# Kernel tuning notes

Measured on AMD Instinct MI355X. Metric: run time of the kernel, lower is better.

## Reference

```python
import jax, jax.numpy as jnp
import numpy as np


def _gla_forward(hidden_state, Wq, bq, Wk, bk, Wv, bv, Wg, bg, Wo, bo):
    # hidden_state: (B, T, H)
    q = hidden_state @ Wq + bq                       # (B, T, K)
    k = jax.nn.sigmoid(hidden_state @ Wk + bk)       # (B, T, K)
    g = jax.nn.sigmoid(hidden_state @ Wg + bg)       # (B, T, K)
    v = hidden_state @ Wv + bv                       # (B, T, V)

    B = hidden_state.shape[0]
    K = Wq.shape[1]
    V = Wv.shape[1]
    state0 = jnp.zeros((B, K, V), dtype=hidden_state.dtype)

    def step(state, inp):
        q_t, k_t, g_t, v_t = inp                     # (B,K),(B,K),(B,K),(B,V)
        # state = state * gate[..., None] + k outer v
        state = state * g_t[:, :, None] + k_t[:, :, None] * v_t[:, None, :]
        out_t = jnp.einsum('bkv,bk->bv', state, q_t)  # (B, V)
        return state, out_t

    # scan over time: move T to leading axis
    xs = (jnp.swapaxes(q, 0, 1), jnp.swapaxes(k, 0, 1),
          jnp.swapaxes(g, 0, 1), jnp.swapaxes(v, 0, 1))
    final_state, outs = jax.lax.scan(step, state0, xs)  # outs: (T, B, V)
    out = jnp.swapaxes(outs, 0, 1)                      # (B, T, V)
    out = out @ Wo + bo                                 # (B, T, O)
    return out, final_state


def setup_inputs() -> dict:
    key = jax.random.key(0)
    ks = jax.random.split(key, 12)
    B, T, H, K, V, O = 8, 2048, 1024, 256, 256, 1024
    s = 0.02
    return {
        'hidden_state': jax.random.normal(ks[0], (B, T, H), dtype=jnp.float32),
        'Wq': jax.random.normal(ks[1], (H, K), dtype=jnp.float32) * s,
        'bq': jax.random.normal(ks[2], (K,), dtype=jnp.float32) * s,
        'Wk': jax.random.normal(ks[3], (H, K), dtype=jnp.float32) * s,
        'bk': jax.random.normal(ks[4], (K,), dtype=jnp.float32) * s,
        'Wv': jax.random.normal(ks[5], (H, V), dtype=jnp.float32) * s,
        'bv': jax.random.normal(ks[6], (V,), dtype=jnp.float32) * s,
        'Wg': jax.random.normal(ks[7], (H, K), dtype=jnp.float32) * s,
        'bg': jax.random.normal(ks[8], (K,), dtype=jnp.float32) * s,
        'Wo': jax.random.normal(ks[9], (V, O), dtype=jnp.float32) * s,
        'bo': jax.random.normal(ks[10], (O,), dtype=jnp.float32) * s,
    }


def reference(hidden_state, Wq, bq, Wk, bk, Wv, bv, Wg, bg, Wo, bo):
    return _gla_forward(hidden_state, Wq, bq, Wk, bk, Wv, bv, Wg, bg, Wo, bo)
```

## Files before the change

kernel.cpp:

```cpp
#include <hip/hip_runtime.h>

#define Bb 8
#define Tt 2048
#define Hh 1024
#define Kk 256
#define Vv 256
#define Oo 1024
#define CC 64
#define NC 32

typedef __attribute__((ext_vector_type(8))) __bf16 bf16x8;
typedef __attribute__((ext_vector_type(4))) float f32x4;

__device__ __forceinline__ unsigned short f2b(float f) {
  unsigned u = __float_as_uint(f);
  u = (u + 0x7FFFu + ((u >> 16) & 1u)) >> 16;
  return (unsigned short)u;
}
__device__ __forceinline__ float b2f(unsigned short u) {
  return __uint_as_float(((unsigned)u) << 16);
}
__device__ __forceinline__ void gload_lds16(const unsigned short* g, unsigned short* l) {
  __builtin_amdgcn_global_load_lds(
      (const __attribute__((address_space(1))) void*)g,
      (__attribute__((address_space(3))) void*)l, 16, 0, 0);
}

__global__ __launch_bounds__(256) void cast_bf16_kernel(const float* __restrict__ in,
                                                        unsigned short* __restrict__ out,
                                                        int n4) {
  int i = blockIdx.x * 256 + threadIdx.x;
  if (i >= n4) return;
  float4 v = ((const float4*)in)[i];
  ushort4 o;
  o.x = f2b(v.x); o.y = f2b(v.y); o.z = f2b(v.z); o.w = f2b(v.w);
  ((ushort4*)out)[i] = o;
}

__global__ __launch_bounds__(256) void transpose_cast_kernel(const float* __restrict__ W,
                                                             unsigned short* __restrict__ WT,
                                                             int H, int N) {
  __shared__ float tile[32][33];
  int h0 = blockIdx.x * 32, n0 = blockIdx.y * 32;
  int tx = threadIdx.x & 31, ty = threadIdx.x >> 5;
  for (int r = ty; r < 32; r += 8)
    tile[r][tx] = W[(size_t)(h0 + r) * N + n0 + tx];
  __syncthreads();
  for (int r = ty; r < 32; r += 8)
    WT[(size_t)(n0 + r) * H + h0 + tx] = f2b(tile[tx][r]);
}

__global__ __launch_bounds__(256) void transpose_b16_kernel(
    const unsigned short* __restrict__ in, unsigned short* __restrict__ out,
    int R, int C) {
  __shared__ unsigned short tile[32][33];
  const int r0 = blockIdx.x * 32, c0 = blockIdx.y * 32;
  const size_t base = (size_t)blockIdx.z * R * C;
  const int tx = threadIdx.x & 31, ty = threadIdx.x >> 5;
  for (int rr = ty; rr < 32; rr += 8)
    tile[rr][tx] = in[base + (size_t)(r0 + rr) * C + c0 + tx];
  __syncthreads();
  for (int rr = ty; rr < 32; rr += 8)
    out[base + (size_t)(c0 + rr) * R + r0 + tx] = tile[tx][rr];
}

#define BM 128
#define BN 128
#define BK 64

template <int MODE>
__global__ __launch_bounds__(256, 4) void gemm_mf_kernel(
    const unsigned short* __restrict__ A, const unsigned short* __restrict__ Bt,
    const float* __restrict__ b0p, const float* __restrict__ b1p,
    const float* __restrict__ b2p, const float* __restrict__ b3p,
    float* __restrict__ Cf,
    unsigned short* __restrict__ O0, unsigned short* __restrict__ O1,
    unsigned short* __restrict__ O2, unsigned short* __restrict__ O3,
    int M, int N, int K) {
  __shared__ __align__(16) unsigned short As[BM * BK];
  __shared__ __align__(16) unsigned short Bs[BN * BK];
  const int tid = threadIdx.x;
  const int lane = tid & 63, wid = tid >> 6;
  const int wm = wid >> 1, wn = wid & 1;
  const int lin = blockIdx.x + blockIdx.y * gridDim.x;
  const int cpx = (gridDim.x * gridDim.y) >> 3;
  const int swz = (lin & 7) * cpx + (lin >> 3);
  const int m0 = (swz / gridDim.x) * BM, n0 = (swz % gridDim.x) * BN;
  const int fr = lane & 15, fq = lane >> 4;
  const int srl = lane >> 3;
  const int scs = ((lane & 7) ^ srl) * 8;
  const unsigned short* gaBase = A + (size_t)(m0 + srl) * K + scs;
  const unsigned short* gbBase = Bt + (size_t)(n0 + srl) * K + scs;

  f32x4 acc[4][4] = {};
  const int nt = K / BK;
  for (int t = 0; t < nt; ++t) {
    const int k0 = t * BK;
    __syncthreads();
#pragma unroll
    for (int inst = 0; inst < 4; ++inst) {
      const int rb = wid * 32 + inst * 8;
      gload_lds16(gaBase + (size_t)rb * K + k0, &As[rb * BK]);
      gload_lds16(gbBase + (size_t)rb * K + k0, &Bs[rb * BK]);
    }
    __syncthreads();
#pragma unroll
    for (int ks = 0; ks < 2; ++ks) {
      bf16x8 af[4], bfv[4];
#pragma unroll
      for (int j = 0; j < 4; ++j) {
        const int R = wn * 64 + j * 16 + fr;
        const int ch = ((ks << 2) | fq) ^ (fr & 7);
        bfv[j] = *(const bf16x8*)&Bs[R * BK + ch * 8];
      }
#pragma unroll
      for (int i = 0; i < 4; ++i) {
        const int R = wm * 64 + i * 16 + fr;
        const int ch = ((ks << 2) | fq) ^ (fr & 7);
        af[i] = *(const bf16x8*)&As[R * BK + ch * 8];
      }
#pragma unroll
      for (int i = 0; i < 4; ++i)
#pragma unroll
        for (int j = 0; j < 4; ++j)
          acc[i][j] = __builtin_amdgcn_mfma_f32_16x16x32_bf16(af[i], bfv[j], acc[i][j], 0, 0, 0);
    }
  }
  if (MODE == 1) {
#pragma unroll
    for (int j = 0; j < 4; ++j) {
      const int n = n0 + wn * 64 + j * 16 + fr;
      const float bv = b0p[n];
#pragma unroll
      for (int i = 0; i < 4; ++i) {
        const int mb = m0 + wm * 64 + i * 16 + fq * 4;
#pragma unroll
        for (int r = 0; r < 4; ++r)
          Cf[(size_t)(mb + r) * N + n] = acc[i][j][r] + bv;
      }
    }
  } else {
    const int sel = n0 >> 8;
    const float* bp = sel == 0 ? b0p : sel == 1 ? b1p : sel == 2 ? b2p : b3p;
    unsigned short* Op = sel == 0 ? O0 : sel == 1 ? O1 : sel == 2 ? O2 : O3;
#pragma unroll
    for (int j = 0; j < 4; ++j) {
      const int nl = (n0 + wn * 64 + j * 16 + fr) & 255;
      const float bv = bp[nl];
#pragma unroll
      for (int i = 0; i < 4; ++i) {
        const int mb = m0 + wm * 64 + i * 16 + fq * 4;
#pragma unroll
        for (int r = 0; r < 4; ++r) {
          const int m = mb + r;
          const float x = acc[i][j][r] + bv;
          if (sel == 0) {
            Op[(size_t)m * Kk + nl] = f2b(x);
          } else if (sel == 1) {
            Op[(size_t)m * Kk + nl] = f2b(1.f / (1.f + expf(-x)));
          } else if (sel == 2) {
            float e = exp2f(-x * 1.44269504f);
            float lg = -log2f(1.f + e);
            _Float16 hv = (_Float16)lg;
            unsigned short u;
            __builtin_memcpy(&u, &hv, 2);
            Op[(size_t)m * Kk + nl] = u;
          } else {
            Op[(size_t)m * Vv + nl] = f2b(x);
          }
        }
      }
    }
  }
}

__global__ __launch_bounds__(256) void prep_sgemm_kernel(
    const unsigned short* __restrict__ qb, const unsigned short* __restrict__ kb,
    const unsigned short* __restrict__ lgb, const unsigned short* __restrict__ vTb,
    unsigned short* __restrict__ q2b, unsigned short* __restrict__ qab,
    unsigned short* __restrict__ kab,
    float* __restrict__ LBb, float* __restrict__ Dendb,
    unsigned short* __restrict__ Sb) {
  __shared__ __align__(16) unsigned short khs[256][72];
  const int c = blockIdx.x, b = blockIdx.y;
  const int k = threadIdx.x;
  const int task = b * NC + c;
  const size_t rowbase = ((size_t)b * Tt + (size_t)c * CC) * Kk + k;
  float Ls = 0.f;
  float LBr[4];
#pragma unroll
  for (int gq = 0; gq < 4; ++gq) {
    LBr[gq] = Ls;
#pragma unroll
    for (int tt = 0; tt < 16; ++tt) {
      int t = gq * 16 + tt;
      _Float16 hv;
      __builtin_memcpy(&hv, &lgb[rowbase + (size_t)t * Kk], 2);
      Ls += (float)hv;
    }
  }
  const float Lend = Ls;
#pragma unroll
  for (int gq = 0; gq < 4; ++gq) LBb[(size_t)task * 1024 + gq * 256 + k] = LBr[gq];
  Dendb[task * 256 + k] = exp2f(Lend);
  float L = 0.f;
#pragma unroll
  for (int gq = 0; gq < 4; ++gq) {
    const float LBc = LBr[gq];
    unsigned kw[8];
#pragma unroll
    for (int tt = 0; tt < 16; ++tt) {
      int t = gq * 16 + tt;
      size_t off = rowbase + (size_t)t * Kk;
      _Float16 hv;
      __builtin_memcpy(&hv, &lgb[off], 2);
      L += (float)hv;
      float qv = b2f(qb[off]);
      float kv = b2f(kb[off]);
      q2b[off] = f2b(qv * exp2f(L));
      qab[off] = f2b(qv * exp2f(L - LBc));
      kab[off] = f2b(kv * exp2f(LBc - L));
      unsigned short kh = f2b(kv * exp2f(Lend - L));
      if (tt & 1) kw[tt >> 1] |= ((unsigned)kh) << 16;
      else        kw[tt >> 1] = kh;
    }
    uint4 u0; u0.x = kw[0]; u0.y = kw[1]; u0.z = kw[2]; u0.w = kw[3];
    uint4 u1; u1.x = kw[4]; u1.y = kw[5]; u1.z = kw[6]; u1.w = kw[7];
    *(uint4*)&khs[k][gq * 16] = u0;
    *(uint4*)&khs[k][gq * 16 + 8] = u1;
  }
  __syncthreads();
  const int tid = threadIdx.x, lane = tid & 63, w = tid >> 6;
  const int fr = lane & 15, fq = lane >> 4, fk = fq * 8;
  const unsigned short* vt = vTb + (size_t)b * (Vv * Tt) + (size_t)c * CC;
  for (int vb4 = 0; vb4 < 4; ++vb4) {
    f32x4 acc[4][4] = {};
#pragma unroll
    for (int ks = 0; ks < 2; ++ks) {
      bf16x8 af[4], bf[4];
#pragma unroll
      for (int i = 0; i < 4; ++i)
        af[i] = *(const bf16x8*)&khs[w * 64 + i * 16 + fr][ks * 32 + fk];
#pragma unroll
      for (int j = 0; j < 4; ++j)
        bf[j] = *(const bf16x8*)(vt + (size_t)(vb4 * 64 + j * 16 + fr) * Tt + ks * 32 + fk);
#pragma unroll
      for (int i = 0; i < 4; ++i)
#pragma unroll
        for (int j = 0; j < 4; ++j)
          acc[i][j] = __builtin_amdgcn_mfma_f32_16x16x32_bf16(af[i], bf[j], acc[i][j], 0, 0, 0);
    }
#pragma unroll
    for (int i = 0; i < 4; ++i)
#pragma unroll
      for (int j = 0; j < 4; ++j)
#pragma unroll
        for (int r = 0; r < 4; ++r)
          Sb[(size_t)task * (Kk * Vv) + (size_t)(w * 64 + i * 16 + fq * 4 + r) * Vv +
             vb4 * 64 + j * 16 + fr] = f2b(acc[i][j][r]);
  }
}

__global__ __launch_bounds__(256) void passR_kernel(
    const unsigned short* __restrict__ Sb, const float* __restrict__ Dendb,
    unsigned short* __restrict__ S0Tb, float* __restrict__ state_out) {
  const int vt = blockIdx.x, kt = blockIdx.y, b = blockIdx.z;
  const int tid = threadIdx.x;
  const int kq = tid >> 2;
  const int vq = tid & 3;
  const int vr = tid >> 3;
  const int kqq = tid & 7;
  __shared__ __align__(16) unsigned short Ts[32][72];
  float st[8];
#pragma unroll
  for (int j = 0; j < 8; ++j) st[j] = 0.f;
  for (int c = 0; c < NC; ++c) {
    const int task = b * NC + c;
#pragma unroll
    for (int j = 0; j < 8; ++j) Ts[vq * 8 + j][kq] = f2b(st[j]);
    __syncthreads();
    {
      unsigned short* dst = S0Tb + (size_t)task * (Kk * Vv) +
                            (size_t)(vt * 32 + vr) * Kk + kt * 64 + kqq * 8;
      *(uint4*)dst = *(const uint4*)&Ts[vr][kqq * 8];
    }
    __syncthreads();
    const float d = Dendb[task * 256 + kt * 64 + kq];
    const unsigned short* sp = Sb + (size_t)task * (Kk * Vv) +
                               (size_t)(kt * 64 + kq) * Vv + vt * 32 + vq * 8;
    uint4 raw = *(const uint4*)sp;
    unsigned ws_[4] = {raw.x, raw.y, raw.z, raw.w};
#pragma unroll
    for (int e = 0; e < 4; ++e) {
      float lo = __uint_as_float(ws_[e] << 16);
      float hi = __uint_as_float(ws_[e] & 0xFFFF0000u);
      st[e * 2]     = d * st[e * 2] + lo;
      st[e * 2 + 1] = d * st[e * 2 + 1] + hi;
    }
  }
  float* so = state_out + (size_t)(b * Kk + kt * 64 + kq) * Vv + vt * 32 + vq * 8;
#pragma unroll
  for (int j = 0; j < 8; ++j) so[j] = st[j];
}

__global__ __launch_bounds__(256) void passO_kernel(
    const unsigned short* __restrict__ qab, const unsigned short* __restrict__ kab,
    const unsigned short* __restrict__ q2b, const float* __restrict__ LBb,
    const unsigned short* __restrict__ S0Tb, const unsigned short* __restrict__ vTb,
    unsigned short* __restrict__ attb) {
  const int c = blockIdx.x, b = blockIdx.y;
  const int task = b * NC + c;
  const int tid = threadIdx.x, lane = tid & 63, w = tid >> 6;
  const int fr = lane & 15, fq = lane >> 4, fk = fq * 8;
  __shared__ float LB_s[4][256];
  __shared__ float D_s[6][256];
  __shared__ __align__(16) unsigned short A_s[64][72];
  const size_t tbase = (size_t)task * (CC * Kk);
  for (int idx = tid; idx < 1024; idx += 256) LB_s[idx >> 8][idx & 255] = LBb[(size_t)task * 1024 + idx];
  for (int idx = tid; idx < 64 * 72 / 2; idx += 256) ((unsigned*)A_s)[idx] = 0;
  __syncthreads();
  {
    const int kk = tid;
#pragma unroll
    for (int pi = 0; pi < 6; ++pi) {
      const int I = (pi >= 3) ? 3 : (pi >= 1) ? 2 : 1;
      const int J = pi - (I * (I - 1)) / 2;
      D_s[pi][kk] = exp2f(LB_s[I][kk] - LB_s[J][kk]);
    }
  }
  __syncthreads();
  for (int p = w; p < 10; p += 4) {
    const int I = (p >= 6) ? 3 : (p >= 3) ? 2 : (p >= 1) ? 1 : 0;
    const int J = p - (I * (I + 1)) / 2;
    const int pidx = (I * (I - 1)) / 2 + J;
    f32x4 acc = {0.f, 0.f, 0.f, 0.f};
#pragma unroll
    for (int ks = 0; ks < 8; ++ks) {
      const int k0 = ks * 32 + fk;
      bf16x8 af = *(const bf16x8*)(qab + tbase + (size_t)(I * 16 + fr) * Kk + k0);
      if (I != J) {
#pragma unroll
        for (int e = 0; e < 8; ++e)
          af[e] = (__bf16)((float)af[e] * D_s[pidx][k0 + e]);
      }
      bf16x8 bf = *(const bf16x8*)(kab + tbase + (size_t)(J * 16 + fr) * Kk + k0);
      acc = __builtin_amdgcn_mfma_f32_16x16x32_bf16(af, bf, acc, 0, 0, 0);
    }
#pragma unroll
    for (int r = 0; r < 4; ++r) {
      const int ml = fq * 4 + r, nl = fr;
      bool keep = (I != J) || (nl <= ml);
      A_s[I * 16 + ml][J * 16 + nl] = keep ? f2b(acc[r]) : (unsigned short)0;
    }
  }
  __syncthreads();
  f32x4 acc2[4][4] = {};
  const unsigned short* q2t = q2b + tbase;
  const unsigned short* s0t = S0Tb + (size_t)task * (Kk * Vv);
  const unsigned short* vtp = vTb + (size_t)b * (Vv * Tt) + (size_t)c * CC;
  const int vbase = w * 64;
#pragma unroll
  for (int ks = 0; ks < 8; ++ks) {
    const int k0 = ks * 32 + fk;
    bf16x8 af[4], bf[4];
#pragma unroll
    for (int i = 0; i < 4; ++i) af[i] = *(const bf16x8*)(q2t + (size_t)(i * 16 + fr) * Kk + k0);
#pragma unroll
    for (int j = 0; j < 4; ++j) bf[j] = *(const bf16x8*)(s0t + (size_t)(vbase + j * 16 + fr) * Kk + k0);
#pragma unroll
    for (int i = 0; i < 4; ++i)
#pragma unroll
      for (int j = 0; j < 4; ++j)
        acc2[i][j] = __builtin_amdgcn_mfma_f32_16x16x32_bf16(af[i], bf[j], acc2[i][j], 0, 0, 0);
  }
#pragma unroll
  for (int ks = 0; ks < 2; ++ks) {
    const int s0 = ks * 32 + fk;
    bf16x8 af[4], bf[4];
#pragma unroll
    for (int i = 0; i < 4; ++i) af[i] = *(const bf16x8*)&A_s[i * 16 + fr][s0];
#pragma unroll
    for (int j = 0; j < 4; ++j) bf[j] = *(const bf16x8*)(vtp + (size_t)(vbase + j * 16 + fr) * Tt + s0);
#pragma unroll
    for (int i = 0; i < 4; ++i)
#pragma unroll
      for (int j = 0; j < 4; ++j)
        acc2[i][j] = __builtin_amdgcn_mfma_f32_16x16x32_bf16(af[i], bf[j], acc2[i][j], 0, 0, 0);
  }
#pragma unroll
  for (int i = 0; i < 4; ++i)
#pragma unroll
    for (int j = 0; j < 4; ++j)
#pragma unroll
      for (int r = 0; r < 4; ++r)
        attb[((size_t)b * Tt + c * CC + i * 16 + fq * 4 + r) * Vv + vbase + j * 16 + fr]
            = f2b(acc2[i][j][r]);
}

extern "C" void kernel_launch(void* const* d_in, const int* in_sizes, int n_in,
                              void* d_out, int out_size, void* d_ws, size_t ws_size,
                              hipStream_t stream) {
  const float* hs = (const float*)d_in[0];
  const float* Wq = (const float*)d_in[1];
  const float* bq = (const float*)d_in[2];
  const float* Wk = (const float*)d_in[3];
  const float* bk = (const float*)d_in[4];
  const float* Wv = (const float*)d_in[5];
  const float* bv = (const float*)d_in[6];
  const float* Wg = (const float*)d_in[7];
  const float* bg = (const float*)d_in[8];
  const float* Wo = (const float*)d_in[9];
  const float* bo = (const float*)d_in[10];

  float* out = (float*)d_out;
  float* state_out = out + (size_t)Bb * Tt * Oo;

  char* p = (char*)d_ws;
  auto alloc = [&](size_t bytes) {
    char* r = p;
    p += (bytes + 255) & ~(size_t)255;
    return r;
  };
  unsigned short* hsb   = (unsigned short*)alloc((size_t)Bb * Tt * Hh * 2);
  unsigned short* WallT = (unsigned short*)alloc((size_t)1024 * Hh * 2);
  unsigned short* WoT   = (unsigned short*)alloc((size_t)Oo * Vv * 2);
  unsigned short* qb    = (unsigned short*)alloc((size_t)Bb * Tt * Kk * 2);
  unsigned short* kb    = (unsigned short*)alloc((size_t)Bb * Tt * Kk * 2);
  unsigned short* lgb   = (unsigned short*)alloc((size_t)Bb * Tt * Kk * 2);
  unsigned short* vb    = (unsigned short*)alloc((size_t)Bb * Tt * Vv * 2);
  unsigned short* vTb   = (unsigned short*)alloc((size_t)Bb * Vv * Tt * 2);
  unsigned short* attb  = (unsigned short*)alloc((size_t)Bb * Tt * Vv * 2);
  unsigned short* q2b   = (unsigned short*)alloc((size_t)Bb * Tt * Kk * 2);
  unsigned short* qab   = (unsigned short*)alloc((size_t)Bb * Tt * Kk * 2);
  unsigned short* kab   = (unsigned short*)alloc((size_t)Bb * Tt * Kk * 2);
  float*          LBb   = (float*)alloc((size_t)Bb * NC * 4 * Kk * 4);
  float*          Dendb = (float*)alloc((size_t)Bb * NC * Kk * 4);
  unsigned short* Sb    = (unsigned short*)alloc((size_t)Bb * NC * Kk * Vv * 2);
  unsigned short* S0Tb  = (unsigned short*)alloc((size_t)Bb * NC * Kk * Vv * 2);

  int n4 = Bb * Tt * Hh / 4;
  cast_bf16_kernel<<<(n4 + 255) / 256, 256, 0, stream>>>(hs, hsb, n4);
  transpose_cast_kernel<<<dim3(Hh / 32, Kk / 32), 256, 0, stream>>>(Wq, WallT + 0 * Kk * Hh, Hh, Kk);
  transpose_cast_kernel<<<dim3(Hh / 32, Kk / 32), 256, 0, stream>>>(Wk, WallT + 1 * Kk * Hh, Hh, Kk);
  transpose_cast_kernel<<<dim3(Hh / 32, Kk / 32), 256, 0, stream>>>(Wg, WallT + 2 * Kk * Hh, Hh, Kk);
  transpose_cast_kernel<<<dim3(Hh / 32, Kk / 32), 256, 0, stream>>>(Wv, WallT + 3 * Kk * Hh, Hh, Kk);
  transpose_cast_kernel<<<dim3(Vv / 32, Oo / 32), 256, 0, stream>>>(Wo, WoT, Vv, Oo);

  gemm_mf_kernel<0><<<dim3(1024 / BN, (Bb * Tt) / BM), 256, 0, stream>>>(
      hsb, WallT, bq, bk, bg, bv, nullptr, qb, kb, lgb, vb, Bb * Tt, 1024, Hh);

  transpose_b16_kernel<<<dim3(Tt / 32, Vv / 32, Bb), 256, 0, stream>>>(vb, vTb, Tt, Vv);

  prep_sgemm_kernel<<<dim3(NC, Bb), 256, 0, stream>>>(qb, kb, lgb, vTb, q2b, qab, kab,
                                                      LBb, Dendb, Sb);

  passR_kernel<<<dim3(Vv / 32, Kk / 64, Bb), 256, 0, stream>>>(Sb, Dendb, S0Tb, state_out);

  passO_kernel<<<dim3(NC, Bb), 256, 0, stream>>>(qab, kab, q2b, LBb, S0Tb, vTb, attb);

  gemm_mf_kernel<1><<<dim3(Oo / BN, (Bb * Tt) / BM), 256, 0, stream>>>(
      attb, WoT, bo, nullptr, nullptr, nullptr, out, nullptr, nullptr, nullptr, nullptr,
      Bb * Tt, Oo, Vv);
}
```

Baseline: 239.9 us.

## Fuse V transpose into projection GEMM epilogue via LDS-staged coalesced stores

The projection GEMM epilogue now stages its bf16 tile in LDS, with the V section written transposed. It then emits 16-byte coalesced stores, writing vT directly and removing the separate transpose kernel and the intermediate v buffer. The other outputs also get vectorized stores instead of scattered 2-byte writes. The block-to-tile swizzle is changed to group M rows per XCD. It adds two barriers and LDS reuse in the epilogue.

```diff
diff --git a/kernel.cpp b/kernel.cpp
--- a/kernel.cpp
+++ b/kernel.cpp
@@ -50,20 +50,6 @@
     WT[(size_t)(n0 + r) * H + h0 + tx] = f2b(tile[tx][r]);
 }
 
-__global__ __launch_bounds__(256) void transpose_b16_kernel(
-    const unsigned short* __restrict__ in, unsigned short* __restrict__ out,
-    int R, int C) {
-  __shared__ unsigned short tile[32][33];
-  const int r0 = blockIdx.x * 32, c0 = blockIdx.y * 32;
-  const size_t base = (size_t)blockIdx.z * R * C;
-  const int tx = threadIdx.x & 31, ty = threadIdx.x >> 5;
-  for (int rr = ty; rr < 32; rr += 8)
-    tile[rr][tx] = in[base + (size_t)(r0 + rr) * C + c0 + tx];
-  __syncthreads();
-  for (int rr = ty; rr < 32; rr += 8)
-    out[base + (size_t)(c0 + rr) * R + r0 + tx] = tile[tx][rr];
-}
-
 #define BM 128
 #define BN 128
 #define BK 64
@@ -77,15 +63,18 @@
     unsigned short* __restrict__ O0, unsigned short* __restrict__ O1,
     unsigned short* __restrict__ O2, unsigned short* __restrict__ O3,
     int M, int N, int K) {
-  __shared__ __align__(16) unsigned short As[BM * BK];
-  __shared__ __align__(16) unsigned short Bs[BN * BK];
+  __shared__ __align__(16) unsigned short shbuf[16384];
+  unsigned short* As = shbuf;
+  unsigned short* Bs = shbuf + 8192;
   const int tid = threadIdx.x;
   const int lane = tid & 63, wid = tid >> 6;
   const int wm = wid >> 1, wn = wid & 1;
   const int lin = blockIdx.x + blockIdx.y * gridDim.x;
-  const int cpx = (gridDim.x * gridDim.y) >> 3;
-  const int swz = (lin & 7) * cpx + (lin >> 3);
-  const int m0 = (swz / gridDim.x) * BM, n0 = (swz % gridDim.x) * BN;
+  const int xcd = lin & 7;
+  const int jj = lin >> 3;
+  const int mpg = gridDim.y >> 3;
+  const int m0 = (xcd * mpg + jj / gridDim.x) * BM;
+  const int n0 = (jj % gridDim.x) * BN;
   const int fr = lane & 15, fq = lane >> 4;
   const int srl = lane >> 3;
   const int scs = ((lane & 7) ^ srl) * 8;
@@ -140,35 +129,63 @@
       }
     }
   } else {
+    __syncthreads();
     const int sel = n0 >> 8;
     const float* bp = sel == 0 ? b0p : sel == 1 ? b1p : sel == 2 ? b2p : b3p;
-    unsigned short* Op = sel == 0 ? O0 : sel == 1 ? O1 : sel == 2 ? O2 : O3;
 #pragma unroll
     for (int j = 0; j < 4; ++j) {
-      const int nl = (n0 + wn * 64 + j * 16 + fr) & 255;
-      const float bv = bp[nl];
+      const int ncol = wn * 64 + j * 16 + fr;
+      const int nloc = (n0 & 255) + ncol;
+      const float bv = bp[nloc];
 #pragma unroll
       for (int i = 0; i < 4; ++i) {
-        const int mb = m0 + wm * 64 + i * 16 + fq * 4;
 #pragma unroll
         for (int r = 0; r < 4; ++r) {
-          const int m = mb + r;
+          const int ml = wm * 64 + i * 16 + fq * 4 + r;
           const float x = acc[i][j][r] + bv;
+          unsigned short us;
           if (sel == 0) {
-            Op[(size_t)m * Kk + nl] = f2b(x);
+            us = f2b(x);
           } else if (sel == 1) {
-            Op[(size_t)m * Kk + nl] = f2b(1.f / (1.f + expf(-x)));
+            us = f2b(1.f / (1.f + expf(-x)));
           } else if (sel == 2) {
             float e = exp2f(-x * 1.44269504f);
             float lg = -log2f(1.f + e);
             _Float16 hv = (_Float16)lg;
-            unsigned short u;
-            __builtin_memcpy(&u, &hv, 2);
-            Op[(size_t)m * Kk + nl] = u;
+            __builtin_memcpy(&us, &hv, 2);
           } else {
-            Op[(size_t)m * Vv + nl] = f2b(x);
+            us = f2b(x);
+          }
+          if (sel == 3) {
+            const int cm = (ml >> 3) ^ (ncol & 15);
+            shbuf[ncol * 128 + cm * 8 + (ml & 7)] = us;
+          } else {
+            const int cn = (ncol >> 3) ^ (ml & 15);
+            shbuf[ml * 128 + cn * 8 + (ncol & 7)] = us;
           }
         }
+      }
+    }
+    __syncthreads();
+    const int row = tid >> 1;
+    const int half = tid & 1;
+    if (sel == 3) {
+      unsigned short* dst = O3 + ((size_t)(m0 >> 11) * Vv + (n0 & 255) + row) * Tt +
+                            (m0 & 2047) + half * 64;
+#pragma unroll
+      for (int ic = 0; ic < 8; ++ic) {
+        const int chunk = half * 8 + ic;
+        const int sc = chunk ^ (row & 15);
+        *(uint4*)(dst + ic * 8) = *(const uint4*)&shbuf[row * 128 + sc * 8];
+      }
+    } else {
+      unsigned short* Op = sel == 0 ? O0 : sel == 1 ? O1 : O2;
+      unsigned short* dst = Op + (size_t)(m0 + row) * 256 + (n0 & 255) + half * 64;
+#pragma unroll
+      for (int ic = 0; ic < 8; ++ic) {
+        const int chunk = half * 8 + ic;
+        const int sc = chunk ^ (row & 15);
+        *(uint4*)(dst + ic * 8) = *(const uint4*)&shbuf[row * 128 + sc * 8];
       }
     }
   }
@@ -427,7 +444,6 @@
   unsigned short* qb    = (unsigned short*)alloc((size_t)Bb * Tt * Kk * 2);
   unsigned short* kb    = (unsigned short*)alloc((size_t)Bb * Tt * Kk * 2);
   unsigned short* lgb   = (unsigned short*)alloc((size_t)Bb * Tt * Kk * 2);
-  unsigned short* vb    = (unsigned short*)alloc((size_t)Bb * Tt * Vv * 2);
   unsigned short* vTb   = (unsigned short*)alloc((size_t)Bb * Vv * Tt * 2);
   unsigned short* attb  = (unsigned short*)alloc((size_t)Bb * Tt * Vv * 2);
   unsigned short* q2b   = (unsigned short*)alloc((size_t)Bb * Tt * Kk * 2);
@@ -447,9 +463,7 @@
   transpose_cast_kernel<<<dim3(Vv / 32, Oo / 32), 256, 0, stream>>>(Wo, WoT, Vv, Oo);
 
   gemm_mf_kernel<0><<<dim3(1024 / BN, (Bb * Tt) / BM), 256, 0, stream>>>(
-      hsb, WallT, bq, bk, bg, bv, nullptr, qb, kb, lgb, vb, Bb * Tt, 1024, Hh);
-
-  transpose_b16_kernel<<<dim3(Tt / 32, Vv / 32, Bb), 256, 0, stream>>>(vb, vTb, Tt, Vv);
+      hsb, WallT, bq, bk, bg, bv, nullptr, qb, kb, lgb, vTb, Bb * Tt, 1024, Hh);
 
   prep_sgemm_kernel<<<dim3(NC, Bb), 256, 0, stream>>>(qb, kb, lgb, vTb, q2b, qab, kab,
                                                       LBb, Dendb, Sb);
```

Result: faster. 218.5 us (median of 2 runs) (-8.9%).
